# Performance work log

Measured on AMD Instinct MI355X. Metric: run time of the kernel, lower is better.

Reference implementation:

```python
import jax, jax.numpy as jnp
import numpy as np

N = 100000      # nodes
E = 3200000     # edges (before self loops)
IN, H, OUT = 512, 256, 64
K = 10
TEMP = 1.5
EPS = 1e-5


def setup_inputs() -> dict:
    key = jax.random.key(0)
    ks = jax.random.split(key, 16)
    def lin(k, fan_in, fan_out):
        lim = 1.0 / np.sqrt(fan_in)
        kw, kb = jax.random.split(k)
        w = jax.random.uniform(kw, (fan_in, fan_out), jnp.float32, -lim, lim)
        b = jax.random.uniform(kb, (fan_out,), jnp.float32, -lim, lim)
        return w, b
    w1, b1 = lin(ks[0], IN, H)
    w2, b2 = lin(ks[1], H, H)
    w3, b3 = lin(ks[2], H, H)
    w4, b4 = lin(ks[3], H, OUT)
    return {
        "x": jax.random.normal(ks[4], (N, IN), jnp.float32),
        "edge_index": jax.random.randint(ks[5], (2, E), 0, N, jnp.int64),
        "w1": w1, "b1": b1, "g1": jnp.ones((H,), jnp.float32), "be1": jnp.zeros((H,), jnp.float32),
        "w2": w2, "b2": b2, "g2": jnp.ones((H,), jnp.float32), "be2": jnp.zeros((H,), jnp.float32),
        "w3": w3, "b3": b3, "g3": jnp.ones((H,), jnp.float32), "be3": jnp.zeros((H,), jnp.float32),
        "w4": w4, "b4": b4,
        "alpha": jnp.full((K + 1,), 1.0 / (K + 1), jnp.float32),
    }


def _bn(h, g, b):
    # batch-statistics BatchNorm1d (training-mode normalization, biased var)
    m = h.mean(axis=0)
    v = ((h - m) ** 2).mean(axis=0)
    return g * (h - m) * jax.lax.rsqrt(v + EPS) + b


def reference(x, edge_index, w1, b1, g1, be1, w2, b2, g2, be2,
              w3, b3, g3, be3, w4, b4, alpha):
    n = x.shape[0]
    # add self loops
    loop = jnp.arange(n, dtype=edge_index.dtype)
    row = jnp.concatenate([edge_index[0], loop])
    col = jnp.concatenate([edge_index[1], loop])
    # symmetric normalization D^{-1/2} A D^{-1/2} (degree counted on row)
    deg = jax.ops.segment_sum(jnp.ones_like(row, x.dtype), row, num_segments=n)
    dinv = jnp.where(deg > 0, jax.lax.rsqrt(deg), 0.0)
    norm = dinv[row] * dinv[col]  # [E+N]

    gelu = lambda h: jax.nn.gelu(h, approximate=False)
    x0 = gelu(_bn(x @ w1 + b1, g1, be1))
    x1 = gelu(_bn(x0 @ w2 + b2, g2, be2) + x0)   # dropout=identity (eval)
    x2 = gelu(_bn(x1 @ w3 + b3, g3, be3) + x1)
    h = x2 @ w4 + b4                              # [N, OUT]

    def step(carry, a):
        xt, acc = carry
        xt = jax.ops.segment_sum(norm[:, None] * xt[col], row, num_segments=n)
        return (xt, acc + a * xt), None

    (_, acc), _ = jax.lax.scan(step, (h, alpha[0] * h), alpha[1:])
    return acc / TEMP
```

## Files before the change

### kernel.cpp

```cpp
#include <hip/hip_runtime.h>
#include <math.h>

#define N_NODES 100000
#define N_IN 512
#define N_H 256
#define N_OUT 64
#define KHOP 10
#define EPS_BN 1e-5f
#define INV_TEMP (1.0f/1.5f)

using half8  = __attribute__((ext_vector_type(8))) _Float16;
using half4  = __attribute__((ext_vector_type(4))) _Float16;
using floatx4 = __attribute__((ext_vector_type(4))) float;

struct ZPtrs { const _Float16* p[KHOP]; };


__global__ void init_kernel(int* __restrict__ cnt, float* __restrict__ sums, int n) {
    int i = blockIdx.x * blockDim.x + threadIdx.x;
    if (i < n) cnt[i] = 0;
    if (i < 2 * N_H) sums[i] = 0.f;
}

__global__ __launch_bounds__(256) void fused_pre_kernel(
    const int* __restrict__ ei, int* __restrict__ cnt, unsigned short* __restrict__ pos,
    const float* __restrict__ w1, _Float16* __restrict__ w1T,
    const float* __restrict__ w2, _Float16* __restrict__ w2T,
    const float* __restrict__ w3, _Float16* __restrict__ w3T,
    const float* __restrict__ w4, _Float16* __restrict__ w4T,
    int E, int nbE) {
    int bid = blockIdx.x;
    int t = threadIdx.x;
    if (bid < nbE) {
        int i = bid * 256 + t;
        if (i < E) {
            int r = ei[i];
            pos[i] = (unsigned short)atomicAdd(&cnt[r], 1);
        }
        return;
    }
    bid -= nbE;
    if (bid < 512) {
        int i = bid * 256 + t;
        int k = i >> 8, n = i & 255;
        w1T[(size_t)n * 512 + k] = (_Float16)w1[i];
        return;
    }
    bid -= 512;
    if (bid < 256) {
        int i = bid * 256 + t;
        int k = i >> 8, n = i & 255;
        w2T[(size_t)n * 256 + k] = (_Float16)w2[i];
        return;
    }
    bid -= 256;
    if (bid < 256) {
        int i = bid * 256 + t;
        int k = i >> 8, n = i & 255;
        w3T[(size_t)n * 256 + k] = (_Float16)w3[i];
        return;
    }
    bid -= 256;
    {
        int i = bid * 256 + t;
        int k = i >> 6, n = i & 63;
        w4T[(size_t)n * 256 + k] = (_Float16)w4[i];
    }
}

__global__ void scan1_kernel(const int* __restrict__ cnt, int* __restrict__ excl,
                             int* __restrict__ bsum, int n) {
    __shared__ int sd[256];
    int t = threadIdx.x;
    int base = blockIdx.x * 1024 + t * 4;
    int v0 = (base + 0 < n) ? cnt[base + 0] + 1 : 0;
    int v1 = (base + 1 < n) ? cnt[base + 1] + 1 : 0;
    int v2 = (base + 2 < n) ? cnt[base + 2] + 1 : 0;
    int v3 = (base + 3 < n) ? cnt[base + 3] + 1 : 0;
    int tot = v0 + v1 + v2 + v3;
    sd[t] = tot;
    __syncthreads();
    for (int off = 1; off < 256; off <<= 1) {
        int x = (t >= off) ? sd[t - off] : 0;
        __syncthreads();
        sd[t] += x;
        __syncthreads();
    }
    int run = sd[t] - tot;
    if (t == 255) bsum[blockIdx.x] = sd[t];
    if (base + 0 < n) excl[base + 0] = run; run += v0;
    if (base + 1 < n) excl[base + 1] = run; run += v1;
    if (base + 2 < n) excl[base + 2] = run; run += v2;
    if (base + 3 < n) excl[base + 3] = run;
}

__global__ void scan2_kernel(int* __restrict__ bsum, int nb) {
    __shared__ int sd[128];
    int t = threadIdx.x;
    int v = (t < nb) ? bsum[t] : 0;
    sd[t] = v;
    __syncthreads();
    for (int off = 1; off < 128; off <<= 1) {
        int x = (t >= off) ? sd[t - off] : 0;
        __syncthreads();
        sd[t] += x;
        __syncthreads();
    }
    if (t < nb) bsum[t] = sd[t] - v;
}

__global__ void scan3_kernel(int* __restrict__ row_ptr, const int* __restrict__ bsum,
                             const int* __restrict__ cnt, float* __restrict__ dinv,
                             float* __restrict__ dinv2, float* __restrict__ sqd,
                             int* __restrict__ colv, int n, int total) {
    int i = blockIdx.x * blockDim.x + threadIdx.x;
    if (i < n) {
        int rp = row_ptr[i] + bsum[i >> 10];
        row_ptr[i] = rp;
        int cv = cnt[i];
        float d = (float)(cv + 1);
        dinv[i]  = rsqrtf(d);
        dinv2[i] = 1.0f / d;
        sqd[i]   = sqrtf(d);
        colv[rp + cv] = i;
    }
    if (i == 0) row_ptr[n] = total;
}

__global__ void fill_kernel(const int* __restrict__ ei, const unsigned short* __restrict__ pos,
                            const int* __restrict__ row_ptr,
                            int* __restrict__ colv, int E, int r0, int r1) {
    int i = blockIdx.x * blockDim.x + threadIdx.x;
    if (i >= E) return;
    int r = ei[i];
    if (r < r0 || r >= r1) return;
    colv[row_ptr[r] + pos[i]] = ei[E + i];
}


#define GELU(u) (0.5f * (u) * (1.f + erff((u) * 0.70710678118654752f)))

template<int KDIM, int NDIM, int BN, int AMODE, bool STATS, bool WRITE_X, bool WRITE_Z, typename CT>
__global__ __launch_bounds__(256) void gemm_mfma_kernel(
    const void* __restrict__ Araw, const _Float16* __restrict__ BT,
    const float* __restrict__ bias, CT* __restrict__ C, int M,
    float* __restrict__ sums, const float* __restrict__ ab,
    const _Float16* __restrict__ res, _Float16* __restrict__ xout,
    const float* __restrict__ dinv, _Float16* __restrict__ z0) {
    constexpr int BM = 128;
    constexpr int LDK = 40;
    constexpr int WTN = BN / 32;
    __shared__ _Float16 As[BM * LDK];
    __shared__ _Float16 Bs[BN * LDK];
    __shared__ float cs[BN];
    __shared__ float cq[BN];
    int t = threadIdx.x;
    int mbase = blockIdx.y * BM;
    int nbase = blockIdx.x * BN;
    int wv = t >> 6, lane = t & 63;
    int wm = (wv & 1) * 64;
    int wn = (wv >> 1) * (BN / 2);
    int q = lane >> 4;
    int fr = lane & 15;
    int sr = t >> 2;
    int sc = (t & 3) * 8;
    bool xwrite = WRITE_X && (blockIdx.x == 0);

    floatx4 acc[4][WTN];
    for (int mt = 0; mt < 4; ++mt)
        for (int nt = 0; nt < WTN; ++nt)
            acc[mt][nt] = floatx4{0.f, 0.f, 0.f, 0.f};

    for (int k0 = 0; k0 < KDIM; k0 += 32) {
        int kc = k0 + sc;
        #pragma unroll
        for (int p = 0; p < 2; ++p) {
            int row = sr + p * 64;
            int grow = mbase + row;
            half8 v = {};
            if (grow < M) {
                if constexpr (AMODE == 0) {
                    v = *reinterpret_cast<const half8*>(
                        &((const _Float16*)Araw)[(size_t)grow * KDIM + kc]);
                } else if constexpr (AMODE == 1) {
                    const float* Af = (const float*)Araw + (size_t)grow * KDIM + kc;
                    float4 f0 = *reinterpret_cast<const float4*>(Af);
                    float4 f1 = *reinterpret_cast<const float4*>(Af + 4);
                    v[0] = (_Float16)f0.x; v[1] = (_Float16)f0.y;
                    v[2] = (_Float16)f0.z; v[3] = (_Float16)f0.w;
                    v[4] = (_Float16)f1.x; v[5] = (_Float16)f1.y;
                    v[6] = (_Float16)f1.z; v[7] = (_Float16)f1.w;
                } else {
                    half8 tv = *reinterpret_cast<const half8*>(
                        &((const _Float16*)Araw)[(size_t)grow * KDIM + kc]);
                    float4 a0 = *reinterpret_cast<const float4*>(&ab[kc]);
                    float4 a1 = *reinterpret_cast<const float4*>(&ab[kc + 4]);
                    float4 b0 = *reinterpret_cast<const float4*>(&ab[KDIM + kc]);
                    float4 b1 = *reinterpret_cast<const float4*>(&ab[KDIM + kc + 4]);
                    float u[8];
                    u[0] = a0.x * (float)tv[0] + b0.x;
                    u[1] = a0.y * (float)tv[1] + b0.y;
                    u[2] = a0.z * (float)tv[2] + b0.z;
                    u[3] = a0.w * (float)tv[3] + b0.w;
                    u[4] = a1.x * (float)tv[4] + b1.x;
                    u[5] = a1.y * (float)tv[5] + b1.y;
                    u[6] = a1.z * (float)tv[6] + b1.z;
                    u[7] = a1.w * (float)tv[7] + b1.w;
                    if constexpr (AMODE == 3) {
                        half8 rv = *reinterpret_cast<const half8*>(
                            &res[(size_t)grow * KDIM + kc]);
                        #pragma unroll
                        for (int j = 0; j < 8; ++j) u[j] += (float)rv[j];
                    }
                    #pragma unroll
                    for (int j = 0; j < 8; ++j) v[j] = (_Float16)GELU(u[j]);
                    if (xwrite)
                        *reinterpret_cast<half8*>(&xout[(size_t)grow * KDIM + kc]) = v;
                }
            }
            *reinterpret_cast<half8*>(&As[row * LDK + sc]) = v;
        }
        #pragma unroll
        for (int p = 0; p < BN / 64; ++p) {
            int row = sr + p * 64;
            half8 v = *reinterpret_cast<const half8*>(&BT[(size_t)(nbase + row) * KDIM + kc]);
            *reinterpret_cast<half8*>(&Bs[row * LDK + sc]) = v;
        }
        __syncthreads();
        half8 af[4], bf[WTN];
        #pragma unroll
        for (int mt = 0; mt < 4; ++mt)
            af[mt] = *reinterpret_cast<const half8*>(&As[(wm + mt * 16 + fr) * LDK + q * 8]);
        #pragma unroll
        for (int nt = 0; nt < WTN; ++nt)
            bf[nt] = *reinterpret_cast<const half8*>(&Bs[(wn + nt * 16 + fr) * LDK + q * 8]);
        #pragma unroll
        for (int mt = 0; mt < 4; ++mt)
            #pragma unroll
            for (int nt = 0; nt < WTN; ++nt)
                acc[mt][nt] = __builtin_amdgcn_mfma_f32_16x16x32_f16(af[mt], bf[nt], acc[mt][nt], 0, 0, 0);
        __syncthreads();
    }
    if constexpr (STATS) {
        if (t < BN) { cs[t] = 0.f; cq[t] = 0.f; }
        __syncthreads();
    }
    #pragma unroll
    for (int nt = 0; nt < WTN; ++nt) {
        int col = nbase + wn + nt * 16 + fr;
        float bv = bias[col];
        float s = 0.f, s2 = 0.f;
        #pragma unroll
        for (int mt = 0; mt < 4; ++mt) {
            #pragma unroll
            for (int rr = 0; rr < 4; ++rr) {
                int row = mbase + wm + mt * 16 + q * 4 + rr;
                if (row < M) {
                    float v = acc[mt][nt][rr] + bv;
                    C[(size_t)row * NDIM + col] = (CT)v;
                    if constexpr (STATS) { s += v; s2 += v * v; }
                    if constexpr (WRITE_Z)
                        z0[((size_t)row << 6) + col] = (_Float16)(dinv[row] * v);
                }
            }
        }
        if constexpr (STATS) {
            s  += __shfl_xor(s, 16);  s  += __shfl_xor(s, 32);
            s2 += __shfl_xor(s2, 16); s2 += __shfl_xor(s2, 32);
            if (q == 0) {
                atomicAdd(&cs[wn + nt * 16 + fr], s);
                atomicAdd(&cq[wn + nt * 16 + fr], s2);
            }
        }
    }
    if constexpr (STATS) {
        __syncthreads();
        if (t < BN) {
            atomicAdd(&sums[nbase + t], cs[t]);
            atomicAdd(&sums[N_H + nbase + t], cq[t]);
        }
    }
}


__global__ void finalize_stats_kernel(float* __restrict__ sums,
                                      const float* __restrict__ g, const float* __restrict__ be,
                                      float* __restrict__ ab, float invM) {
    int c = threadIdx.x;
    float s = sums[c], s2 = sums[N_H + c];
    float mean = s * invM;
    float var = s2 * invM - mean * mean;
    float a = g[c] * rsqrtf(var + EPS_BN);
    ab[c] = a;
    ab[N_H + c] = be[c] - mean * a;
    sums[c] = 0.f;
    sums[N_H + c] = 0.f;
}


__global__ __launch_bounds__(256) void prop_kernel(
    const _Float16* __restrict__ zin, _Float16* __restrict__ zout,
    const int* __restrict__ colv, const int* __restrict__ row_ptr,
    const float* __restrict__ dinv2, int n) {
    int r = (blockIdx.x << 2) + (threadIdx.x >> 6);
    if (r >= n) return;
    int lane = threadIdx.x & 63;
    int esub = lane >> 4;
    int fo = (lane & 15) << 2;
    int s = __builtin_amdgcn_readfirstlane(row_ptr[r]);
    int e = __builtin_amdgcn_readfirstlane(row_ptr[r + 1]);
    float a0 = 0.f, a1 = 0.f, a2 = 0.f, a3 = 0.f;
    int i = s;
    for (; i + 16 <= e; i += 16) {
        int c0 = colv[i + esub];
        int c1 = colv[i + 4 + esub];
        int c2 = colv[i + 8 + esub];
        int c3 = colv[i + 12 + esub];
        half4 v0 = *reinterpret_cast<const half4*>(&zin[((size_t)c0 << 6) + fo]);
        half4 v1 = *reinterpret_cast<const half4*>(&zin[((size_t)c1 << 6) + fo]);
        half4 v2 = *reinterpret_cast<const half4*>(&zin[((size_t)c2 << 6) + fo]);
        half4 v3 = *reinterpret_cast<const half4*>(&zin[((size_t)c3 << 6) + fo]);
        a0 += (float)v0.x + (float)v1.x + (float)v2.x + (float)v3.x;
        a1 += (float)v0.y + (float)v1.y + (float)v2.y + (float)v3.y;
        a2 += (float)v0.z + (float)v1.z + (float)v2.z + (float)v3.z;
        a3 += (float)v0.w + (float)v1.w + (float)v2.w + (float)v3.w;
    }
    for (; i + 4 <= e; i += 4) {
        int c = colv[i + esub];
        half4 v = *reinterpret_cast<const half4*>(&zin[((size_t)c << 6) + fo]);
        a0 += (float)v.x; a1 += (float)v.y; a2 += (float)v.z; a3 += (float)v.w;
    }
    int rem = e - i;
    if (esub < rem) {
        int c = colv[i + esub];
        half4 v = *reinterpret_cast<const half4*>(&zin[((size_t)c << 6) + fo]);
        a0 += (float)v.x; a1 += (float)v.y; a2 += (float)v.z; a3 += (float)v.w;
    }
    a0 += __shfl_xor(a0, 16); a1 += __shfl_xor(a1, 16);
    a2 += __shfl_xor(a2, 16); a3 += __shfl_xor(a3, 16);
    a0 += __shfl_xor(a0, 32); a1 += __shfl_xor(a1, 32);
    a2 += __shfl_xor(a2, 32); a3 += __shfl_xor(a3, 32);
    if (lane < 16) {
        float d = dinv2[r];
        half4 o;
        o.x = (_Float16)(a0 * d); o.y = (_Float16)(a1 * d);
        o.z = (_Float16)(a2 * d); o.w = (_Float16)(a3 * d);
        *reinterpret_cast<half4*>(&zout[((size_t)r << 6) + fo]) = o;
    }
}

__global__ void prop_final_kernel(const float* __restrict__ h, ZPtrs zp,
                                  const float* __restrict__ sqd,
                                  const float* __restrict__ alpha,
                                  float* __restrict__ out, int total4) {
    int i = blockIdx.x * blockDim.x + threadIdx.x;
    if (i >= total4) return;
    int r = i >> 4;
    float4 hv = reinterpret_cast<const float4*>(h)[i];
    float s0 = 0.f, s1 = 0.f, s2 = 0.f, s3 = 0.f;
    #pragma unroll
    for (int k = 0; k < KHOP; ++k) {
        half4 z = reinterpret_cast<const half4*>(zp.p[k])[i];
        float ak = alpha[k + 1];
        s0 += ak * (float)z.x; s1 += ak * (float)z.y;
        s2 += ak * (float)z.z; s3 += ak * (float)z.w;
    }
    float sq = sqd[r];
    float a0 = alpha[0];
    float4 o;
    o.x = INV_TEMP * (a0 * hv.x + sq * s0);
    o.y = INV_TEMP * (a0 * hv.y + sq * s1);
    o.z = INV_TEMP * (a0 * hv.z + sq * s2);
    o.w = INV_TEMP * (a0 * hv.w + sq * s3);
    reinterpret_cast<float4*>(out)[i] = o;
}


extern "C" void kernel_launch(void* const* d_in, const int* in_sizes, int n_in,
                              void* d_out, int out_size, void* d_ws, size_t ws_size,
                              hipStream_t stream) {
    const float* x    = (const float*)d_in[0];
    const int*   ei   = (const int*)d_in[1];
    const float* w1   = (const float*)d_in[2];
    const float* b1   = (const float*)d_in[3];
    const float* g1   = (const float*)d_in[4];
    const float* be1  = (const float*)d_in[5];
    const float* w2   = (const float*)d_in[6];
    const float* b2   = (const float*)d_in[7];
    const float* g2   = (const float*)d_in[8];
    const float* be2  = (const float*)d_in[9];
    const float* w3   = (const float*)d_in[10];
    const float* b3   = (const float*)d_in[11];
    const float* g3   = (const float*)d_in[12];
    const float* be3  = (const float*)d_in[13];
    const float* w4   = (const float*)d_in[14];
    const float* b4   = (const float*)d_in[15];
    const float* alpha= (const float*)d_in[16];
    float* out = (float*)d_out;

    const int N = in_sizes[0] / N_IN;
    const int E = in_sizes[1] / 2;
    const int EN = E + N;
    const size_t NZ = (size_t)N * N_OUT;

    char* ws = (char*)d_ws;
    size_t off = 0;
    auto alloc = [&](size_t bytes) -> void* {
        void* p = ws + off;
        off = (off + bytes + 255) & ~(size_t)255;
        return p;
    };
    int*   cnt     = (int*)alloc((size_t)N * 4);
    int*   row_ptr = (int*)alloc((size_t)(N + 1) * 4);
    float* dinv    = (float*)alloc((size_t)N * 4);
    float* dinv2   = (float*)alloc((size_t)N * 4);
    float* sqd     = (float*)alloc((size_t)N * 4);
    int*   colv    = (int*)alloc((size_t)EN * 4);
    unsigned short* pos = (unsigned short*)alloc((size_t)E * 2);
    int*   bsum    = (int*)alloc(128 * 4);
    float* sums    = (float*)alloc(2 * N_H * 4);
    float* ab      = (float*)alloc(2 * N_H * 4);
    _Float16* w1T  = (_Float16*)alloc((size_t)N_IN * N_H * 2);
    _Float16* w2T  = (_Float16*)alloc((size_t)N_H * N_H * 2);
    _Float16* w3T  = (_Float16*)alloc((size_t)N_H * N_H * 2);
    _Float16* w4T  = (_Float16*)alloc((size_t)N_H * N_OUT * 2);
    float* T       = (float*)alloc((size_t)N * N_H * 4);
    _Float16* Ah0  = (_Float16*)alloc((size_t)N * N_H * 2);
    _Float16* Ah1  = (_Float16*)alloc((size_t)N * N_H * 2);
    float* hbuf    = (float*)alloc((size_t)N * N_OUT * 4);
    _Float16* z0   = (_Float16*)alloc(NZ * 2);

    _Float16* T16a = (_Float16*)T;
    _Float16* T16b = (_Float16*)T + (size_t)N * N_H;

    _Float16* zk[KHOP + 1];
    zk[0] = z0;
    for (int k = 1; k <= 8; ++k) zk[k] = (_Float16*)T + (size_t)(k - 1) * NZ;
    zk[9]  = (_Float16*)Ah1;
    zk[10] = (_Float16*)Ah1 + NZ;

    const int TB = 256;
    int nbN  = (N + TB - 1) / TB;
    int nbE  = (E + TB - 1) / TB;
    int nscan = (N + 1023) / 1024;

    init_kernel<<<nbN, TB, 0, stream>>>(cnt, sums, N);
    {
        int grid = nbE + 512 + 256 + 256 + 64;
        fused_pre_kernel<<<grid, TB, 0, stream>>>(ei, cnt, pos,
                                                  w1, w1T, w2, w2T, w3, w3T, w4, w4T,
                                                  E, nbE);
    }

    scan1_kernel<<<nscan, TB, 0, stream>>>(cnt, row_ptr, bsum, N);
    scan2_kernel<<<1, 128, 0, stream>>>(bsum, nscan);
    scan3_kernel<<<nbN, TB, 0, stream>>>(row_ptr, bsum, cnt, dinv, dinv2, sqd, colv, N, EN);

    {
        const int P = 4;
        int step = (N + P - 1) / P;
        for (int p = 0; p < P; ++p) {
            int r0 = p * step;
            int r1 = min(N, r0 + step);
            fill_kernel<<<nbE, TB, 0, stream>>>(ei, pos, row_ptr, colv, E, r0, r1);
        }
    }

    int mt = (N + 127) / 128;

    gemm_mfma_kernel<N_IN, N_H, 128, 1, true, false, false, _Float16>
        <<<dim3(N_H / 128, mt), TB, 0, stream>>>(
        x, w1T, b1, T16a, N, sums, nullptr, nullptr, nullptr, nullptr, nullptr);
    finalize_stats_kernel<<<1, N_H, 0, stream>>>(sums, g1, be1, ab, 1.0f / N);
    gemm_mfma_kernel<N_H, N_H, 128, 2, true, true, false, _Float16>
        <<<dim3(N_H / 128, mt), TB, 0, stream>>>(
        T16a, w2T, b2, T16b, N, sums, ab, nullptr, Ah0, nullptr, nullptr);
    finalize_stats_kernel<<<1, N_H, 0, stream>>>(sums, g2, be2, ab, 1.0f / N);
    gemm_mfma_kernel<N_H, N_H, 128, 3, true, true, false, _Float16>
        <<<dim3(N_H / 128, mt), TB, 0, stream>>>(
        T16b, w3T, b3, T16a, N, sums, ab, Ah0, Ah1, nullptr, nullptr);
    finalize_stats_kernel<<<1, N_H, 0, stream>>>(sums, g3, be3, ab, 1.0f / N);
    gemm_mfma_kernel<N_H, N_OUT, 64, 3, false, false, true, float>
        <<<dim3(1, mt), TB, 0, stream>>>(
        T16a, w4T, b4, hbuf, N, nullptr, ab, Ah1, nullptr, dinv, z0);

    int nbProp = (N + 3) / 4;
    for (int k = 1; k <= KHOP; ++k) {
        prop_kernel<<<nbProp, TB, 0, stream>>>(zk[k - 1], zk[k], colv, row_ptr, dinv2, N);
    }

    ZPtrs zp;
    for (int k = 0; k < KHOP; ++k) zp.p[k] = zk[k + 1];
    int total4 = N * N_OUT / 4;
    prop_final_kernel<<<(total4 + TB - 1) / TB, TB, 0, stream>>>(hbuf, zp, sqd, alpha, out, total4);
}
```

Measured before the change: 1.542 ms.

## Tile SpMM propagation by source-column ranges to improve gather cache locality

Builds a CSR with per-row sub-segments for four column tiles and runs each propagation hop as four passes, one per tile, accumulating fp32 partials in a scratch buffer. The intent is to keep the gathered source slice cache-resident and reduce random-gather misses. In exchange it adds fp32 partial read/write traffic per pass, four times the launches and row-pointer loads, and fewer edges per row per pass, which weakens latency hiding.

```diff
diff --git a/kernel.cpp b/kernel.cpp
--- a/kernel.cpp
+++ b/kernel.cpp
@@ -8,6 +8,7 @@
 #define KHOP 10
 #define EPS_BN 1e-5f
 #define INV_TEMP (1.0f/1.5f)
+#define TILE_W 25000
 
 using half8  = __attribute__((ext_vector_type(8))) _Float16;
 using half4  = __attribute__((ext_vector_type(4))) _Float16;
@@ -16,14 +17,14 @@
 struct ZPtrs { const _Float16* p[KHOP]; };
 
 
-__global__ void init_kernel(int* __restrict__ cnt, float* __restrict__ sums, int n) {
+__global__ void init_kernel(int* __restrict__ cnt4, float* __restrict__ sums, int n4) {
     int i = blockIdx.x * blockDim.x + threadIdx.x;
-    if (i < n) cnt[i] = 0;
+    if (i < n4) cnt4[i] = 0;
     if (i < 2 * N_H) sums[i] = 0.f;
 }
 
 __global__ __launch_bounds__(256) void fused_pre_kernel(
-    const int* __restrict__ ei, int* __restrict__ cnt, unsigned short* __restrict__ pos,
+    const int* __restrict__ ei, int* __restrict__ cnt4, unsigned short* __restrict__ pos,
     const float* __restrict__ w1, _Float16* __restrict__ w1T,
     const float* __restrict__ w2, _Float16* __restrict__ w2T,
     const float* __restrict__ w3, _Float16* __restrict__ w3T,
@@ -35,7 +36,8 @@
         int i = bid * 256 + t;
         if (i < E) {
             int r = ei[i];
-            pos[i] = (unsigned short)atomicAdd(&cnt[r], 1);
+            int c = ei[E + i];
+            pos[i] = (unsigned short)atomicAdd(&cnt4[(r << 2) + c / TILE_W], 1);
         }
         return;
     }
@@ -68,15 +70,16 @@
     }
 }
 
-__global__ void scan1_kernel(const int* __restrict__ cnt, int* __restrict__ excl,
-                             int* __restrict__ bsum, int n) {
+__global__ void scan1_kernel(const int* __restrict__ cnt4, int* __restrict__ excl,
+                             int* __restrict__ bsum, int n4) {
     __shared__ int sd[256];
     int t = threadIdx.x;
     int base = blockIdx.x * 1024 + t * 4;
-    int v0 = (base + 0 < n) ? cnt[base + 0] + 1 : 0;
-    int v1 = (base + 1 < n) ? cnt[base + 1] + 1 : 0;
-    int v2 = (base + 2 < n) ? cnt[base + 2] + 1 : 0;
-    int v3 = (base + 3 < n) ? cnt[base + 3] + 1 : 0;
+    int v0 = 0, v1 = 0, v2 = 0, v3 = 0;
+    if (base + 0 < n4) { int g = base + 0; v0 = cnt4[g] + (((g & 3) == ((g >> 2) / TILE_W)) ? 1 : 0); }
+    if (base + 1 < n4) { int g = base + 1; v1 = cnt4[g] + (((g & 3) == ((g >> 2) / TILE_W)) ? 1 : 0); }
+    if (base + 2 < n4) { int g = base + 2; v2 = cnt4[g] + (((g & 3) == ((g >> 2) / TILE_W)) ? 1 : 0); }
+    if (base + 3 < n4) { int g = base + 3; v3 = cnt4[g] + (((g & 3) == ((g >> 2) / TILE_W)) ? 1 : 0); }
     int tot = v0 + v1 + v2 + v3;
     sd[t] = tot;
     __syncthreads();
@@ -88,19 +91,19 @@
     }
     int run = sd[t] - tot;
     if (t == 255) bsum[blockIdx.x] = sd[t];
-    if (base + 0 < n) excl[base + 0] = run; run += v0;
-    if (base + 1 < n) excl[base + 1] = run; run += v1;
-    if (base + 2 < n) excl[base + 2] = run; run += v2;
-    if (base + 3 < n) excl[base + 3] = run;
+    if (base + 0 < n4) excl[base + 0] = run; run += v0;
+    if (base + 1 < n4) excl[base + 1] = run; run += v1;
+    if (base + 2 < n4) excl[base + 2] = run; run += v2;
+    if (base + 3 < n4) excl[base + 3] = run;
 }
 
 __global__ void scan2_kernel(int* __restrict__ bsum, int nb) {
-    __shared__ int sd[128];
+    __shared__ int sd[512];
     int t = threadIdx.x;
     int v = (t < nb) ? bsum[t] : 0;
     sd[t] = v;
     __syncthreads();
-    for (int off = 1; off < 128; off <<= 1) {
+    for (int off = 1; off < 512; off <<= 1) {
         int x = (t >= off) ? sd[t - off] : 0;
         __syncthreads();
         sd[t] += x;
@@ -109,32 +112,37 @@
     if (t < nb) bsum[t] = sd[t] - v;
 }
 
-__global__ void scan3_kernel(int* __restrict__ row_ptr, const int* __restrict__ bsum,
-                             const int* __restrict__ cnt, float* __restrict__ dinv,
+__global__ void scan3_kernel(int* __restrict__ rp4, const int* __restrict__ bsum,
+                             const int* __restrict__ cnt4, float* __restrict__ dinv,
                              float* __restrict__ dinv2, float* __restrict__ sqd,
-                             int* __restrict__ colv, int n, int total) {
-    int i = blockIdx.x * blockDim.x + threadIdx.x;
-    if (i < n) {
-        int rp = row_ptr[i] + bsum[i >> 10];
-        row_ptr[i] = rp;
-        int cv = cnt[i];
-        float d = (float)(cv + 1);
-        dinv[i]  = rsqrtf(d);
-        dinv2[i] = 1.0f / d;
-        sqd[i]   = sqrtf(d);
-        colv[rp + cv] = i;
-    }
-    if (i == 0) row_ptr[n] = total;
+                             int* __restrict__ colv, int n4, int total) {
+    int g = blockIdx.x * blockDim.x + threadIdx.x;
+    if (g < n4) {
+        int rpf = rp4[g] + bsum[g >> 10];
+        rp4[g] = rpf;
+        int r = g >> 2, t = g & 3;
+        int cv = cnt4[g];
+        if (t == r / TILE_W) colv[rpf + cv] = r;
+        if (t == 0) {
+            int4 c4 = *reinterpret_cast<const int4*>(&cnt4[g]);
+            float d = (float)(c4.x + c4.y + c4.z + c4.w + 1);
+            dinv[r]  = rsqrtf(d);
+            dinv2[r] = 1.0f / d;
+            sqd[r]   = sqrtf(d);
+        }
+    }
+    if (g == 0) rp4[n4] = total;
 }
 
 __global__ void fill_kernel(const int* __restrict__ ei, const unsigned short* __restrict__ pos,
-                            const int* __restrict__ row_ptr,
+                            const int* __restrict__ rp4,
                             int* __restrict__ colv, int E, int r0, int r1) {
     int i = blockIdx.x * blockDim.x + threadIdx.x;
     if (i >= E) return;
     int r = ei[i];
     if (r < r0 || r >= r1) return;
-    colv[row_ptr[r] + pos[i]] = ei[E + i];
+    int c = ei[E + i];
+    colv[rp4[(r << 2) + c / TILE_W] + pos[i]] = c;
 }
 
 
@@ -298,40 +306,37 @@
 }
 
 
-__global__ __launch_bounds__(256) void prop_kernel(
-    const _Float16* __restrict__ zin, _Float16* __restrict__ zout,
-    const int* __restrict__ colv, const int* __restrict__ row_ptr,
-    const float* __restrict__ dinv2, int n) {
-    int r = (blockIdx.x << 2) + (threadIdx.x >> 6);
+template<int PHASE>
+__global__ __launch_bounds__(1024) void prop_tile_kernel(
+    const _Float16* __restrict__ zin, float* __restrict__ zpart,
+    _Float16* __restrict__ zout,
+    const int* __restrict__ colv, const int* __restrict__ rp4,
+    const float* __restrict__ dinv2, int n, int tile) {
+    int r = (blockIdx.x << 4) + (threadIdx.x >> 6);
     if (r >= n) return;
     int lane = threadIdx.x & 63;
     int esub = lane >> 4;
     int fo = (lane & 15) << 2;
-    int s = __builtin_amdgcn_readfirstlane(row_ptr[r]);
-    int e = __builtin_amdgcn_readfirstlane(row_ptr[r + 1]);
+    int s = __builtin_amdgcn_readfirstlane(rp4[(r << 2) + tile]);
+    int e = __builtin_amdgcn_readfirstlane(rp4[(r << 2) + tile + 1]);
     float a0 = 0.f, a1 = 0.f, a2 = 0.f, a3 = 0.f;
     int i = s;
-    for (; i + 16 <= e; i += 16) {
+    for (; i + 8 <= e; i += 8) {
         int c0 = colv[i + esub];
         int c1 = colv[i + 4 + esub];
-        int c2 = colv[i + 8 + esub];
-        int c3 = colv[i + 12 + esub];
         half4 v0 = *reinterpret_cast<const half4*>(&zin[((size_t)c0 << 6) + fo]);
         half4 v1 = *reinterpret_cast<const half4*>(&zin[((size_t)c1 << 6) + fo]);
-        half4 v2 = *reinterpret_cast<const half4*>(&zin[((size_t)c2 << 6) + fo]);
-        half4 v3 = *reinterpret_cast<const half4*>(&zin[((size_t)c3 << 6) + fo]);
-        a0 += (float)v0.x + (float)v1.x + (float)v2.x + (float)v3.x;
-        a1 += (float)v0.y + (float)v1.y + (float)v2.y + (float)v3.y;
-        a2 += (float)v0.z + (float)v1.z + (float)v2.z + (float)v3.z;
-        a3 += (float)v0.w + (float)v1.w + (float)v2.w + (float)v3.w;
+        a0 += (float)v0.x + (float)v1.x;
+        a1 += (float)v0.y + (float)v1.y;
+        a2 += (float)v0.z + (float)v1.z;
+        a3 += (float)v0.w + (float)v1.w;
     }
     for (; i + 4 <= e; i += 4) {
         int c = colv[i + esub];
         half4 v = *reinterpret_cast<const half4*>(&zin[((size_t)c << 6) + fo]);
         a0 += (float)v.x; a1 += (float)v.y; a2 += (float)v.z; a3 += (float)v.w;
     }
-    int rem = e - i;
-    if (esub < rem) {
+    if (esub < e - i) {
         int c = colv[i + esub];
         half4 v = *reinterpret_cast<const half4*>(&zin[((size_t)c << 6) + fo]);
         a0 += (float)v.x; a1 += (float)v.y; a2 += (float)v.z; a3 += (float)v.w;
@@ -341,11 +346,21 @@
     a0 += __shfl_xor(a0, 32); a1 += __shfl_xor(a1, 32);
     a2 += __shfl_xor(a2, 32); a3 += __shfl_xor(a3, 32);
     if (lane < 16) {
-        float d = dinv2[r];
-        half4 o;
-        o.x = (_Float16)(a0 * d); o.y = (_Float16)(a1 * d);
-        o.z = (_Float16)(a2 * d); o.w = (_Float16)(a3 * d);
-        *reinterpret_cast<half4*>(&zout[((size_t)r << 6) + fo]) = o;
+        float4* zp = reinterpret_cast<float4*>(&zpart[((size_t)r << 6) + fo]);
+        if constexpr (PHASE == 0) {
+            *zp = float4{a0, a1, a2, a3};
+        } else if constexpr (PHASE == 1) {
+            float4 p = *zp;
+            p.x += a0; p.y += a1; p.z += a2; p.w += a3;
+            *zp = p;
+        } else {
+            float4 p = *zp;
+            float d = dinv2[r];
+            half4 o;
+            o.x = (_Float16)((a0 + p.x) * d); o.y = (_Float16)((a1 + p.y) * d);
+            o.z = (_Float16)((a2 + p.z) * d); o.w = (_Float16)((a3 + p.w) * d);
+            *reinterpret_cast<half4*>(&zout[((size_t)r << 6) + fo]) = o;
+        }
     }
 }
 
@@ -401,7 +416,9 @@
     const int N = in_sizes[0] / N_IN;
     const int E = in_sizes[1] / 2;
     const int EN = E + N;
+    const int N4 = N * 4;
     const size_t NZ = (size_t)N * N_OUT;
+    const int NT = (N + TILE_W - 1) / TILE_W;
 
     char* ws = (char*)d_ws;
     size_t off = 0;
@@ -410,14 +427,14 @@
         off = (off + bytes + 255) & ~(size_t)255;
         return p;
     };
-    int*   cnt     = (int*)alloc((size_t)N * 4);
-    int*   row_ptr = (int*)alloc((size_t)(N + 1) * 4);
+    int*   cnt4    = (int*)alloc((size_t)N4 * 4);
+    int*   rp4     = (int*)alloc((size_t)(N4 + 1) * 4);
     float* dinv    = (float*)alloc((size_t)N * 4);
     float* dinv2   = (float*)alloc((size_t)N * 4);
     float* sqd     = (float*)alloc((size_t)N * 4);
     int*   colv    = (int*)alloc((size_t)EN * 4);
     unsigned short* pos = (unsigned short*)alloc((size_t)E * 2);
-    int*   bsum    = (int*)alloc(128 * 4);
+    int*   bsum    = (int*)alloc(512 * 4);
     float* sums    = (float*)alloc(2 * N_H * 4);
     float* ab      = (float*)alloc(2 * N_H * 4);
     _Float16* w1T  = (_Float16*)alloc((size_t)N_IN * N_H * 2);
@@ -429,6 +446,7 @@
     _Float16* Ah1  = (_Float16*)alloc((size_t)N * N_H * 2);
     float* hbuf    = (float*)alloc((size_t)N * N_OUT * 4);
     _Float16* z0   = (_Float16*)alloc(NZ * 2);
+    float* zpart   = (float*)alloc(NZ * 4);
 
     _Float16* T16a = (_Float16*)T;
     _Float16* T16b = (_Float16*)T + (size_t)N * N_H;
@@ -440,21 +458,21 @@
     zk[10] = (_Float16*)Ah1 + NZ;
 
     const int TB = 256;
-    int nbN  = (N + TB - 1) / TB;
+    int nbN4 = (N4 + TB - 1) / TB;
     int nbE  = (E + TB - 1) / TB;
-    int nscan = (N + 1023) / 1024;
-
-    init_kernel<<<nbN, TB, 0, stream>>>(cnt, sums, N);
+    int nscan = (N4 + 1023) / 1024;
+
+    init_kernel<<<nbN4, TB, 0, stream>>>(cnt4, sums, N4);
     {
         int grid = nbE + 512 + 256 + 256 + 64;
-        fused_pre_kernel<<<grid, TB, 0, stream>>>(ei, cnt, pos,
+        fused_pre_kernel<<<grid, TB, 0, stream>>>(ei, cnt4, pos,
                                                   w1, w1T, w2, w2T, w3, w3T, w4, w4T,
                                                   E, nbE);
     }
 
-    scan1_kernel<<<nscan, TB, 0, stream>>>(cnt, row_ptr, bsum, N);
-    scan2_kernel<<<1, 128, 0, stream>>>(bsum, nscan);
-    scan3_kernel<<<nbN, TB, 0, stream>>>(row_ptr, bsum, cnt, dinv, dinv2, sqd, colv, N, EN);
+    scan1_kernel<<<nscan, TB, 0, stream>>>(cnt4, rp4, bsum, N4);
+    scan2_kernel<<<1, 512, 0, stream>>>(bsum, nscan);
+    scan3_kernel<<<nbN4, TB, 0, stream>>>(rp4, bsum, cnt4, dinv, dinv2, sqd, colv, N4, EN);
 
     {
         const int P = 4;
@@ -462,7 +480,7 @@
         for (int p = 0; p < P; ++p) {
             int r0 = p * step;
             int r1 = min(N, r0 + step);
-            fill_kernel<<<nbE, TB, 0, stream>>>(ei, pos, row_ptr, colv, E, r0, r1);
+            fill_kernel<<<nbE, TB, 0, stream>>>(ei, pos, rp4, colv, E, r0, r1);
         }
     }
 
@@ -484,9 +502,15 @@
         <<<dim3(1, mt), TB, 0, stream>>>(
         T16a, w4T, b4, hbuf, N, nullptr, ab, Ah1, nullptr, dinv, z0);
 
-    int nbProp = (N + 3) / 4;
+    int nbProp = (N + 15) / 16;
     for (int k = 1; k <= KHOP; ++k) {
-        prop_kernel<<<nbProp, TB, 0, stream>>>(zk[k - 1], zk[k], colv, row_ptr, dinv2, N);
+        prop_tile_kernel<0><<<nbProp, 1024, 0, stream>>>(
+            zk[k - 1], zpart, nullptr, colv, rp4, dinv2, N, 0);
+        for (int t = 1; t < NT - 1; ++t)
+            prop_tile_kernel<1><<<nbProp, 1024, 0, stream>>>(
+                zk[k - 1], zpart, nullptr, colv, rp4, dinv2, N, t);
+        prop_tile_kernel<2><<<nbProp, 1024, 0, stream>>>(
+            zk[k - 1], zpart, zk[k], colv, rp4, dinv2, N, NT - 1);
     }
 
     ZPtrs zp;
```

After: 2.523 ms. 1.64x slower.
